# Kernel optimization log

Hardware: AMD Instinct MI355X
Metric: run time of the kernel (lower is better)

The kernel has to match this reference:

```python
import jax, jax.numpy as jnp
import numpy as np

N_QUBITS = 10
DIM = 1 << N_QUBITS
N_PARAMS = 6 * N_QUBITS - 3
W_MUL = (2 ** 0.5) * (5 ** -0.5)  # he_std * lrmul with gain=sqrt(2), use_wscale=True, lrmul=1

_C = jnp.complex64
X = jnp.array([[0, 1], [1, 0]], dtype=_C)
Y = jnp.array([[0, -1j], [1j, 0]], dtype=_C)
Z = jnp.array([[1, 0], [0, -1]], dtype=_C)
XX = jnp.kron(X, X)
YY = jnp.kron(Y, Y)
ZZ = jnp.kron(Z, Z)
CNOT = jnp.array([[1, 0, 0, 0], [0, 1, 0, 0], [0, 0, 0, 1], [0, 0, 1, 0]], dtype=_C)


def _rot(theta, P):
    # exp(-i theta/2 P) for involutory P (X, Y, Z, XX, YY, ZZ)
    th = theta.astype(_C)
    eye = jnp.eye(P.shape[0], dtype=_C)
    return jnp.cos(th / 2) * eye - 1j * jnp.sin(th / 2) * P


def _apply(rho, G, axes):
    # contract k-qubit gate G (2^k x 2^k) onto the given tensor axes of rho
    k = len(axes)
    Gt = G.reshape((2,) * (2 * k))
    rho = jnp.tensordot(Gt, rho, axes=(list(range(k, 2 * k)), list(axes)))
    return jnp.moveaxis(rho, list(range(k)), list(axes))


def _evolve(rho_t, w):
    # rho_t: [B] + [2]*n (row qubits) + [2]*n (col qubits); implements rho -> U rho U^dagger
    n = N_QUBITS
    for q in range(n - 1):
        gates = [_rot(w[3 * q + 0], XX), _rot(w[3 * q + 1], YY), _rot(w[3 * q + 2], ZZ), CNOT]
        for G in gates:
            rho_t = _apply(rho_t, G, (1 + q, 2 + q))            # G on rows
            rho_t = _apply(rho_t, G.conj(), (1 + n + q, 2 + n + q))  # G^dagger on cols
    wl = w[3 * n - 3:]
    for q in range(n):
        # ZYXLayer: rz, ry, rx per wire
        gates = [_rot(wl[3 * q + 0], Z), _rot(wl[3 * q + 1], Y), _rot(wl[3 * q + 2], X)]
        for G in gates:
            rho_t = _apply(rho_t, G, (1 + q,))
            rho_t = _apply(rho_t, G.conj(), (1 + n + q,))
    return rho_t


def setup_inputs() -> dict:
    key = jax.random.key(0)
    k1, k2, k3 = jax.random.split(key, 3)
    B = 16
    return {
        'x_real': jax.random.normal(k1, (B, 1, DIM), dtype=jnp.float32),
        'x_imag': jax.random.normal(k2, (B, 1, DIM), dtype=jnp.float32),
        'weight': jax.random.uniform(k3, (N_PARAMS,), dtype=jnp.float32, minval=0.0, maxval=2 * np.pi),
        'dimA': 5,
    }


def reference(x_real, x_imag, weight, dimA):
    x = (x_real + 1j * x_imag).astype(_C)              # [B, 1, DIM]
    B = x.shape[0]
    w = weight * W_MUL
    rho = jnp.einsum('boi,boj->bij', x, x.conj())      # |x><x| : [B, DIM, DIM]
    rho_t = rho.reshape((B,) + (2,) * (2 * N_QUBITS))
    rho_t = _evolve(rho_t, w)
    rho = rho_t.reshape(B, DIM, DIM)
    dimB = N_QUBITS - dimA
    dA, dB = 1 << dimA, 1 << dimB
    r = rho.reshape(B, dB, dA, dB, dA)
    red = jnp.einsum('biaic->bac', r)                  # partial trace over first dimB qubits
    return red.reshape(B, 1, dA * dA)
```

## Files before the change

### kernel.cpp

```cpp
#include <hip/hip_runtime.h>

#define NQ   10
#define DIM  1024
#define NP   57
#define WMUL 0.6324555320336759f

__device__ __forceinline__ int ixs(int i) { return i ^ ((i >> 4) & 15); }

__device__ __forceinline__ void chain1q(float2& u, float2& v,
    float cz, float sz, float cy, float sy, float cx, float sx)
{
    float tur = cz*u.x + sz*u.y, tui = cz*u.y - sz*u.x;
    float tvr = cz*v.x - sz*v.y, tvi = cz*v.y + sz*v.x;
    float ur = cy*tur - sy*tvr, ui = cy*tui - sy*tvi;
    float vr = sy*tur + cy*tvr, vi = sy*tui + cy*tvi;
    u.x = cx*ur + sx*vi; u.y = cx*ui - sx*vr;
    v.x = cx*vr + sx*ui; v.y = cx*vi - sx*ur;
}

__device__ __forceinline__ void gate2q(float2& A0, float2& A1, float2& A2, float2& A3,
    float c1, float s1, float c2, float s2, float c3, float s3)
{
    float t0r = c1*A0.x + s1*A3.y, t0m = c1*A0.y - s1*A3.x;
    float t3r = c1*A3.x + s1*A0.y, t3m = c1*A3.y - s1*A0.x;
    float t1r = c1*A1.x + s1*A2.y, t1m = c1*A1.y - s1*A2.x;
    float t2r = c1*A2.x + s1*A1.y, t2m = c1*A2.y - s1*A1.x;
    float r0 = c2*t0r - s2*t3m, m0 = c2*t0m + s2*t3r;
    float r3 = c2*t3r - s2*t0m, m3 = c2*t3m + s2*t0r;
    float r1 = c2*t1r + s2*t2m, m1 = c2*t1m - s2*t2r;
    float r2 = c2*t2r + s2*t1m, m2 = c2*t2m - s2*t1r;
    A0.x = c3*r0 + s3*m0; A0.y = c3*m0 - s3*r0;
    A3.x = c3*r3 + s3*m3; A3.y = c3*m3 - s3*r3;
    A1.x = c3*r1 - s3*m1; A1.y = c3*m1 + s3*r1;
    A2.x = c3*r2 - s3*m2; A2.y = c3*m2 + s3*r2;
}

__global__ __launch_bounds__(256) void qupool_sv_kernel(
    const float* __restrict__ xr,
    const float* __restrict__ xi,
    const float* __restrict__ w,
    const int*   __restrict__ dimA_p,
    float* __restrict__ out,
    int out_size)
{
    __shared__ float2 s[DIM];
    __shared__ float sc[NP], ss[NP];

    const int b = blockIdx.x;
    const int t = threadIdx.x;
    const int base = b * DIM;

    float c1, s1, c2, s2, c3, s3;
    {
        float th0 = w[0] * (WMUL * 0.5f);
        float th1 = w[1] * (WMUL * 0.5f);
        float th2 = w[2] * (WMUL * 0.5f);
        sincosf(th0, &s1, &c1);
        sincosf(th1, &s2, &c2);
        sincosf(th2, &s3, &c3);
    }
    if (t < NP) {
        float th = w[t] * (WMUL * 0.5f);
        float sv, cv; sincosf(th, &sv, &cv);
        sc[t] = cv; ss[t] = sv;
    }

    {
        float2 A0 = make_float2(xr[base + t      ], xi[base + t      ]);
        float2 A1 = make_float2(xr[base + t + 256], xi[base + t + 256]);
        float2 A2 = make_float2(xr[base + t + 512], xi[base + t + 512]);
        float2 A3 = make_float2(xr[base + t + 768], xi[base + t + 768]);
        gate2q(A0, A1, A2, A3, c1, s1, c2, s2, c3, s3);
        s[ixs(t      )] = A0;
        s[ixs(t + 256)] = A1;
        s[ixs(t + 512)] = A3;
        s[ixs(t + 768)] = A2;
    }
    __syncthreads();

    #pragma unroll
    for (int q = 1; q < NQ - 1; ++q) {
        const int p  = NQ - 1 - q;
        const int pl = p - 1;
        const float g1c = sc[3*q  ], g1s = ss[3*q  ];
        const float g2c = sc[3*q+1], g2s = ss[3*q+1];
        const float g3c = sc[3*q+2], g3s = ss[3*q+2];

        const int low  = t & ((1 << pl) - 1);
        const int high = t >> pl;
        const int i0   = (high << (p + 1)) | low;
        const int i1   = i0 | (1 << pl);
        const int i2   = i0 | (1 << p);
        const int i3   = i2 | (1 << pl);

        float2 A0 = s[ixs(i0)], A1 = s[ixs(i1)], A2 = s[ixs(i2)], A3 = s[ixs(i3)];
        gate2q(A0, A1, A2, A3, g1c, g1s, g2c, g2s, g3c, g3s);
        s[ixs(i0)] = A0; s[ixs(i1)] = A1;
        s[ixs(i2)] = A3; s[ixs(i3)] = A2;
        __syncthreads();
    }

    #pragma unroll
    for (int j = 0; j < 5; ++j) {
        const int bl = 8 - 2*j;
        const int bh = bl + 1;
        const int kb = 27 + 6*j;
        const float cz0 = sc[kb+0], sz0 = ss[kb+0];
        const float cy0 = sc[kb+1], sy0 = ss[kb+1];
        const float cx0 = sc[kb+2], sx0 = ss[kb+2];
        const float cz1 = sc[kb+3], sz1 = ss[kb+3];
        const float cy1 = sc[kb+4], sy1 = ss[kb+4];
        const float cx1 = sc[kb+5], sx1 = ss[kb+5];

        const int low  = t & ((1 << bl) - 1);
        const int high = t >> bl;
        const int i0   = (high << (bh + 1)) | low;
        const int i1   = i0 | (1 << bl);
        const int i2   = i0 | (1 << bh);
        const int i3   = i2 | (1 << bl);

        float2 A0 = s[ixs(i0)], A1 = s[ixs(i1)], A2 = s[ixs(i2)], A3 = s[ixs(i3)];
        chain1q(A0, A2, cz0, sz0, cy0, sy0, cx0, sx0);
        chain1q(A1, A3, cz0, sz0, cy0, sy0, cx0, sx0);
        chain1q(A0, A1, cz1, sz1, cy1, sy1, cx1, sx1);
        chain1q(A2, A3, cz1, sz1, cy1, sy1, cx1, sx1);
        s[ixs(i0)] = A0; s[ixs(i1)] = A1; s[ixs(i2)] = A2; s[ixs(i3)] = A3;
        __syncthreads();
    }

    const int dimA = dimA_p[0];
    const int dA   = 1 << dimA;
    const int nout = dA * dA;
    const bool cplx = (out_size >= 2 * (int)gridDim.x * nout);

    if (dA == 32) {
        const int c  = t & 31;
        const int a0 = t >> 5;
        float ar[4]  = {0.f, 0.f, 0.f, 0.f};
        float aim[4] = {0.f, 0.f, 0.f, 0.f};
        #pragma unroll 4
        for (int iB = 0; iB < 32; ++iB) {
            const float2 vc = s[ixs(iB*32 + c)];
            #pragma unroll
            for (int k = 0; k < 4; ++k) {
                const float2 va = s[ixs(iB*32 + a0 + 8*k)];
                ar[k]  += va.x*vc.x + va.y*vc.y;
                aim[k] += va.y*vc.x - va.x*vc.y;
            }
        }
        #pragma unroll
        for (int k = 0; k < 4; ++k) {
            const size_t oo = (size_t)b*nout + (t + 256*k);
            if (cplx) { out[2*oo] = ar[k]; out[2*oo+1] = aim[k]; }
            else      { out[oo] = ar[k]; }
        }
    } else {
        const int dB = DIM >> dimA;
        for (int o = t; o < nout; o += 256) {
            const int a = o >> dimA;
            const int c = o & (dA - 1);
            float accr = 0.f, acci = 0.f;
            for (int i = 0; i < dB; ++i) {
                const float2 va = s[ixs(i*dA + a)];
                const float2 vv = s[ixs(i*dA + c)];
                accr += va.x*vv.x + va.y*vv.y;
                acci += va.y*vv.x - va.x*vv.y;
            }
            const size_t oo = (size_t)b*nout + o;
            if (cplx) { out[2*oo] = accr; out[2*oo+1] = acci; }
            else      { out[oo] = accr; }
        }
    }
}

extern "C" void kernel_launch(void* const* d_in, const int* in_sizes, int n_in,
                              void* d_out, int out_size, void* d_ws, size_t ws_size,
                              hipStream_t stream) {
    const float* xr = (const float*)d_in[0];
    const float* xi = (const float*)d_in[1];
    const float* w  = (const float*)d_in[2];
    const int*   dA = (const int*)d_in[3];
    float* out = (float*)d_out;

    const int B = in_sizes[0] / DIM;
    qupool_sv_kernel<<<dim3(B), dim3(256), 0, stream>>>(xr, xi, w, dA, out, out_size);
}
```

Before: 67.23 us.

## Fuse gate layers via warp shuffles to cut shared-memory rounds and barriers

Pairs adjacent two-qubit gate layers into one shared-memory round, using xor-1 lane shuffles to exchange amplitudes between the two gates. The last 2q round also absorbs the final single-qubit chains. The single-qubit layers are grouped four qubits per round, with shuffles transposing data in registers. This cuts the shared-memory read/write/barrier rounds from 14 to 6, at the cost of extra shuffle instructions and more intricate index mapping. The global loads are also hoisted above the sincos setup so they overlap.

```diff
diff --git a/kernel.cpp b/kernel.cpp
--- a/kernel.cpp
+++ b/kernel.cpp
@@ -6,6 +6,13 @@
 #define WMUL 0.6324555320336759f
 
 __device__ __forceinline__ int ixs(int i) { return i ^ ((i >> 4) & 15); }
+
+__device__ __forceinline__ float2 shflx2(float2 v, int m) {
+    float2 r;
+    r.x = __shfl_xor(v.x, m);
+    r.y = __shfl_xor(v.y, m);
+    return r;
+}
 
 __device__ __forceinline__ void chain1q(float2& u, float2& v,
     float cz, float sz, float cy, float sy, float cx, float sx)
@@ -35,6 +42,107 @@
     A2.x = c3*r2 - s3*m2; A2.y = c3*m2 + s3*r2;
 }
 
+template<int B2>
+__device__ __forceinline__ void fused2q_round(float2* __restrict__ s, int t,
+                                              const float* __restrict__ sc,
+                                              const float* __restrict__ ss)
+{
+    constexpr int B1 = B2 - 1, B0 = B2 - 2;
+    constexpr int QA = 9 - B2;
+    const float a1c = sc[3*QA+0], a1s = ss[3*QA+0];
+    const float a2c = sc[3*QA+1], a2s = ss[3*QA+1];
+    const float a3c = sc[3*QA+2], a3s = ss[3*QA+2];
+    const float b1c = sc[3*QA+3], b1s = ss[3*QA+3];
+    const float b2c = sc[3*QA+4], b2s = ss[3*QA+4];
+    const float b3c = sc[3*QA+5], b3s = ss[3*QA+5];
+
+    const int my   = t & 1;
+    const int u    = t >> 1;
+    const int low  = u & ((1 << B0) - 1);
+    const int high = u >> B0;
+    const int rb   = (high << (B2 + 1)) | low | (my << B0);
+
+    float2 A0 = s[ixs(rb)];
+    float2 A1 = s[ixs(rb | (1 << B1))];
+    float2 A2 = s[ixs(rb | (1 << B2))];
+    float2 A3 = s[ixs(rb | (1 << B2) | (1 << B1))];
+    gate2q(A0, A1, A2, A3, a1c, a1s, a2c, a2s, a3c, a3s);
+    float2 B00 = A0, B01 = A1, B10 = A3, B11 = A2;
+
+    float2 snd0 = my ? B00 : B10;
+    float2 snd1 = my ? B01 : B11;
+    float2 rcv0 = shflx2(snd0, 1);
+    float2 rcv1 = shflx2(snd1, 1);
+    float2 kp0  = my ? B10 : B00;
+    float2 kp1  = my ? B11 : B01;
+
+    float2 D00 = my ? rcv0 : kp0;
+    float2 D01 = my ? kp0  : rcv0;
+    float2 D10 = my ? rcv1 : kp1;
+    float2 D11 = my ? kp1  : rcv1;
+    gate2q(D00, D01, D10, D11, b1c, b1s, b2c, b2s, b3c, b3s);
+    float2 E00 = D00, E01 = D01, E10 = D11, E11 = D10;
+
+    if (B2 == 2) {
+        chain1q(E00, E10, sc[51], ss[51], sc[52], ss[52], sc[53], ss[53]);
+        chain1q(E01, E11, sc[51], ss[51], sc[52], ss[52], sc[53], ss[53]);
+        chain1q(E00, E01, sc[54], ss[54], sc[55], ss[55], sc[56], ss[56]);
+        chain1q(E10, E11, sc[54], ss[54], sc[55], ss[55], sc[56], ss[56]);
+    }
+
+    const int wb = (high << (B2 + 1)) | low | (my << B2);
+    s[ixs(wb)]                         = E00;
+    s[ixs(wb | (1 << B0))]             = E01;
+    s[ixs(wb | (1 << B1))]             = E10;
+    s[ixs(wb | (1 << B1) | (1 << B0))] = E11;
+}
+
+template<int CB, int RB, int QH0, int QH1, int QL0, int QL1>
+__device__ __forceinline__ void cluster1q_round(float2* __restrict__ s, int t,
+                                                const float* __restrict__ sc,
+                                                const float* __restrict__ ss)
+{
+    const int c1 = (t >> 1) & 1, c0 = t & 1;
+    const int u  = t >> 2;
+    const int low  = u & ((1 << (RB - 1)) - 1);
+    const int high = u >> (RB - 1);
+    const int ib = (high << (CB + 1)) | (c1 << CB) | (c0 << (CB - 1)) | low;
+
+    float2 F00 = s[ixs(ib)];
+    float2 F01 = s[ixs(ib | (1 << (RB - 1)))];
+    float2 F10 = s[ixs(ib | (1 << RB))];
+    float2 F11 = s[ixs(ib | (1 << RB) | (1 << (RB - 1)))];
+
+    chain1q(F00, F10, sc[27+3*QL0], ss[27+3*QL0], sc[28+3*QL0], ss[28+3*QL0], sc[29+3*QL0], ss[29+3*QL0]);
+    chain1q(F01, F11, sc[27+3*QL0], ss[27+3*QL0], sc[28+3*QL0], ss[28+3*QL0], sc[29+3*QL0], ss[29+3*QL0]);
+    chain1q(F00, F01, sc[27+3*QL1], ss[27+3*QL1], sc[28+3*QL1], ss[28+3*QL1], sc[29+3*QL1], ss[29+3*QL1]);
+    chain1q(F10, F11, sc[27+3*QL1], ss[27+3*QL1], sc[28+3*QL1], ss[28+3*QL1], sc[29+3*QL1], ss[29+3*QL1]);
+
+    {
+        float2 s0 = c1 ? F00 : F10;
+        float2 s1 = c1 ? F01 : F11;
+        float2 g0 = shflx2(s0, 2), g1 = shflx2(s1, 2);
+        if (c1) { F00 = g0; F01 = g1; } else { F10 = g0; F11 = g1; }
+    }
+    {
+        float2 s0 = c0 ? F00 : F01;
+        float2 s1 = c0 ? F10 : F11;
+        float2 g0 = shflx2(s0, 1), g1 = shflx2(s1, 1);
+        if (c0) { F00 = g0; F10 = g1; } else { F01 = g0; F11 = g1; }
+    }
+
+    chain1q(F00, F10, sc[27+3*QH0], ss[27+3*QH0], sc[28+3*QH0], ss[28+3*QH0], sc[29+3*QH0], ss[29+3*QH0]);
+    chain1q(F01, F11, sc[27+3*QH0], ss[27+3*QH0], sc[28+3*QH0], ss[28+3*QH0], sc[29+3*QH0], ss[29+3*QH0]);
+    chain1q(F00, F01, sc[27+3*QH1], ss[27+3*QH1], sc[28+3*QH1], ss[28+3*QH1], sc[29+3*QH1], ss[29+3*QH1]);
+    chain1q(F10, F11, sc[27+3*QH1], ss[27+3*QH1], sc[28+3*QH1], ss[28+3*QH1], sc[29+3*QH1], ss[29+3*QH1]);
+
+    const int jb = (high << (CB + 1)) | (c1 << RB) | (c0 << (RB - 1)) | low;
+    s[ixs(jb)]                              = F00;
+    s[ixs(jb | (1 << (CB - 1)))]            = F01;
+    s[ixs(jb | (1 << CB))]                  = F10;
+    s[ixs(jb | (1 << CB) | (1 << (CB-1)))]  = F11;
+}
+
 __global__ __launch_bounds__(256) void qupool_sv_kernel(
     const float* __restrict__ xr,
     const float* __restrict__ xi,
@@ -50,83 +158,37 @@
     const int t = threadIdx.x;
     const int base = b * DIM;
 
+    float2 A0 = make_float2(xr[base + t      ], xi[base + t      ]);
+    float2 A1 = make_float2(xr[base + t + 256], xi[base + t + 256]);
+    float2 A2 = make_float2(xr[base + t + 512], xi[base + t + 512]);
+    float2 A3 = make_float2(xr[base + t + 768], xi[base + t + 768]);
+
     float c1, s1, c2, s2, c3, s3;
     {
-        float th0 = w[0] * (WMUL * 0.5f);
-        float th1 = w[1] * (WMUL * 0.5f);
-        float th2 = w[2] * (WMUL * 0.5f);
-        sincosf(th0, &s1, &c1);
-        sincosf(th1, &s2, &c2);
-        sincosf(th2, &s3, &c3);
+        float sv, cv;
+        sincosf(w[0] * (WMUL * 0.5f), &sv, &cv); c1 = cv; s1 = sv;
+        sincosf(w[1] * (WMUL * 0.5f), &sv, &cv); c2 = cv; s2 = sv;
+        sincosf(w[2] * (WMUL * 0.5f), &sv, &cv); c3 = cv; s3 = sv;
     }
     if (t < NP) {
-        float th = w[t] * (WMUL * 0.5f);
-        float sv, cv; sincosf(th, &sv, &cv);
+        float sv, cv; sincosf(w[t] * (WMUL * 0.5f), &sv, &cv);
         sc[t] = cv; ss[t] = sv;
     }
 
-    {
-        float2 A0 = make_float2(xr[base + t      ], xi[base + t      ]);
-        float2 A1 = make_float2(xr[base + t + 256], xi[base + t + 256]);
-        float2 A2 = make_float2(xr[base + t + 512], xi[base + t + 512]);
-        float2 A3 = make_float2(xr[base + t + 768], xi[base + t + 768]);
-        gate2q(A0, A1, A2, A3, c1, s1, c2, s2, c3, s3);
-        s[ixs(t      )] = A0;
-        s[ixs(t + 256)] = A1;
-        s[ixs(t + 512)] = A3;
-        s[ixs(t + 768)] = A2;
-    }
+    gate2q(A0, A1, A2, A3, c1, s1, c2, s2, c3, s3);
+    s[ixs(t      )] = A0;
+    s[ixs(t + 256)] = A1;
+    s[ixs(t + 512)] = A3;
+    s[ixs(t + 768)] = A2;
     __syncthreads();
 
-    #pragma unroll
-    for (int q = 1; q < NQ - 1; ++q) {
-        const int p  = NQ - 1 - q;
-        const int pl = p - 1;
-        const float g1c = sc[3*q  ], g1s = ss[3*q  ];
-        const float g2c = sc[3*q+1], g2s = ss[3*q+1];
-        const float g3c = sc[3*q+2], g3s = ss[3*q+2];
-
-        const int low  = t & ((1 << pl) - 1);
-        const int high = t >> pl;
-        const int i0   = (high << (p + 1)) | low;
-        const int i1   = i0 | (1 << pl);
-        const int i2   = i0 | (1 << p);
-        const int i3   = i2 | (1 << pl);
-
-        float2 A0 = s[ixs(i0)], A1 = s[ixs(i1)], A2 = s[ixs(i2)], A3 = s[ixs(i3)];
-        gate2q(A0, A1, A2, A3, g1c, g1s, g2c, g2s, g3c, g3s);
-        s[ixs(i0)] = A0; s[ixs(i1)] = A1;
-        s[ixs(i2)] = A3; s[ixs(i3)] = A2;
-        __syncthreads();
-    }
-
-    #pragma unroll
-    for (int j = 0; j < 5; ++j) {
-        const int bl = 8 - 2*j;
-        const int bh = bl + 1;
-        const int kb = 27 + 6*j;
-        const float cz0 = sc[kb+0], sz0 = ss[kb+0];
-        const float cy0 = sc[kb+1], sy0 = ss[kb+1];
-        const float cx0 = sc[kb+2], sx0 = ss[kb+2];
-        const float cz1 = sc[kb+3], sz1 = ss[kb+3];
-        const float cy1 = sc[kb+4], sy1 = ss[kb+4];
-        const float cx1 = sc[kb+5], sx1 = ss[kb+5];
-
-        const int low  = t & ((1 << bl) - 1);
-        const int high = t >> bl;
-        const int i0   = (high << (bh + 1)) | low;
-        const int i1   = i0 | (1 << bl);
-        const int i2   = i0 | (1 << bh);
-        const int i3   = i2 | (1 << bl);
-
-        float2 A0 = s[ixs(i0)], A1 = s[ixs(i1)], A2 = s[ixs(i2)], A3 = s[ixs(i3)];
-        chain1q(A0, A2, cz0, sz0, cy0, sy0, cx0, sx0);
-        chain1q(A1, A3, cz0, sz0, cy0, sy0, cx0, sx0);
-        chain1q(A0, A1, cz1, sz1, cy1, sy1, cx1, sx1);
-        chain1q(A2, A3, cz1, sz1, cy1, sy1, cx1, sx1);
-        s[ixs(i0)] = A0; s[ixs(i1)] = A1; s[ixs(i2)] = A2; s[ixs(i3)] = A3;
-        __syncthreads();
-    }
+    fused2q_round<8>(s, t, sc, ss);  __syncthreads();
+    fused2q_round<6>(s, t, sc, ss);  __syncthreads();
+    fused2q_round<4>(s, t, sc, ss);  __syncthreads();
+    fused2q_round<2>(s, t, sc, ss);  __syncthreads();
+
+    cluster1q_round<9, 7, 0, 1, 2, 3>(s, t, sc, ss); __syncthreads();
+    cluster1q_round<5, 3, 4, 5, 6, 7>(s, t, sc, ss); __syncthreads();
 
     const int dimA = dimA_p[0];
     const int dA   = 1 << dimA;
```

After: 66.47 us. Within noise of the previous version (-1.1%).
